# Kernel optimization log

Hardware: AMD Instinct MI355X
Metric: run time of the kernel (lower is better)

## Reference

```python
import jax, jax.numpy as jnp
from jax import lax
import numpy as np

CONF_THRESH = 0.015
NMS_DIST = 4
BORDER = 4
RED = 8


def setup_inputs() -> dict:
    key = jax.random.key(0)
    k1, k2, k3, k4, k5 = jax.random.split(key, 5)
    B, C, H, W = 32, 128, 64, 64
    MID, NCLS = 256, RED * RED + 1
    return {
        "x": jax.random.normal(k1, (B, C, H, W), dtype=jnp.float32),
        "w1": jax.random.normal(k2, (MID, C, 3, 3), dtype=jnp.float32) * 0.05,
        "b1": jax.random.normal(k3, (MID,), dtype=jnp.float32) * 0.05,
        "w2": jax.random.normal(k4, (NCLS, MID, 1, 1), dtype=jnp.float32) * 0.05,
        "b2": jax.random.normal(k5, (NCLS,), dtype=jnp.float32) * 0.05,
    }


def _conv3x3(x, w, b):
    y = lax.conv_general_dilated(
        x, w, window_strides=(1, 1), padding="SAME",
        dimension_numbers=("NCHW", "OIHW", "NCHW"))
    return y + b[None, :, None, None]


def _max_pool(s, r):
    # s: [B, H, W]; infinity-norm neighborhood max, window (2r+1)x(2r+1)
    return lax.reduce_window(
        s, -jnp.inf, lax.max,
        window_dimensions=(1, 2 * r + 1, 2 * r + 1),
        window_strides=(1, 1, 1), padding="SAME")


def _grid_nms(scores, r, iters=8):
    # Iterated local-max suppression; converges to the greedy (sorted-by-score)
    # grid NMS of the original nms_fast routine for distinct scores.
    zeros = jnp.zeros_like(scores)
    max_mask = (scores == _max_pool(scores, r)) & (scores > 0)
    for _ in range(iters):
        supp = _max_pool(max_mask.astype(scores.dtype), r) > 0
        supp_scores = jnp.where(supp, zeros, scores)
        new_max = (supp_scores == _max_pool(supp_scores, r)) & (supp_scores > 0)
        max_mask = max_mask | (new_max & ~supp)
    return jnp.where(max_mask, scores, zeros)


def reference(x, w1, b1, w2, b2):
    B, _, hh, ww = x.shape
    h = jax.nn.relu(_conv3x3(x, w1, b1))                       # [B, mid, hh, ww]
    semi = jnp.einsum("bchw,oc->bohw", h, w2[:, :, 0, 0]) + b2[None, :, None, None]
    dense = jax.nn.softmax(semi, axis=1)                        # [B, 65, hh, ww]
    nodust = dense[:, :-1]                                      # drop dust bin
    # depth-to-space: [B,64,hh,ww] -> [B, hh*8, ww*8]
    heat = nodust.transpose(0, 2, 3, 1).reshape(B, hh, ww, RED, RED)
    heat = heat.transpose(0, 1, 3, 2, 4).reshape(B, hh * RED, ww * RED)
    # confidence threshold
    scores = jnp.where(heat >= CONF_THRESH, heat, 0.0)
    # grid-based NMS (dense keep-map formulation of nms_fast)
    kept = _grid_nms(scores, NMS_DIST)
    # border removal
    Hi, Wi = hh * RED, ww * RED
    yy = jnp.arange(Hi)
    xx = jnp.arange(Wi)
    border = ((yy[:, None] >= BORDER) & (yy[:, None] < Hi - BORDER) &
              (xx[None, :] >= BORDER) & (xx[None, :] < Wi - BORDER))
    return kept * border[None, :, :].astype(kept.dtype)
```

## Files before the change

kernel.cpp:

```cpp
#include <hip/hip_runtime.h>
#include <hip/hip_bf16.h>
#include <stdint.h>

#define BATCH 32
#define CIN 128
#define HH 64
#define WW 64
#define MID 256
#define NCLS 65
#define HI 512
#define NWORDS 8
#define XPS 136
#define HBS2 264
#define SEMS 68

typedef _Float16 half8 __attribute__((ext_vector_type(8)));
typedef _Float16 half4v __attribute__((ext_vector_type(4)));
typedef _Float16 half2v __attribute__((ext_vector_type(2)));
typedef float f32x4 __attribute__((ext_vector_type(4)));

__global__ __launch_bounds__(256) void prep_w1f(
    const float* __restrict__ w1, _Float16* __restrict__ w1fh,
    _Float16* __restrict__ w1fl)
{
    const int idx = blockIdx.x * 256 + threadIdx.x;
    const int j = idx & 7, lane = (idx >> 3) & 63, mt = (idx >> 9) & 15;
    const int s = (idx >> 13) & 3, kix = idx >> 15;
    const int m = mt * 16 + (lane & 15);
    const int c = s * 32 + (lane >> 4) * 8 + j;
    const int ky = kix / 3, kx = kix - ky * 3;
    const float v = w1[((m * CIN + c) * 3 + ky) * 3 + kx];
    const _Float16 hi = (_Float16)v;
    w1fh[idx] = hi;
    w1fl[idx] = (_Float16)(v - (float)hi);
}

__global__ __launch_bounds__(256) void prep_w2f(
    const float* __restrict__ w2, _Float16* __restrict__ w2fh,
    _Float16* __restrict__ w2fl)
{
    const int idx = blockIdx.x * 256 + threadIdx.x;
    const int j = idx & 7, lane = (idx >> 3) & 63;
    const int ks = (idx >> 9) & 7, mt = idx >> 12;
    const int o = mt * 16 + (lane & 15);
    const int k = ks * 32 + (lane >> 4) * 8 + j;
    const float v = (o < NCLS) ? w2[o * MID + k] : 0.f;
    const _Float16 hi = (_Float16)v;
    w2fh[idx] = hi;
    w2fl[idx] = (_Float16)(v - (float)hi);
}

__global__ __launch_bounds__(256) void head_kernel(
    const float* __restrict__ x,
    const _Float16* __restrict__ w1fh, const _Float16* __restrict__ w1fl,
    const _Float16* __restrict__ w2fh, const _Float16* __restrict__ w2fl,
    const float* __restrict__ b1, const float* __restrict__ b2,
    float* __restrict__ out)
{
    const int b  = blockIdx.z;
    const int y0 = blockIdx.y * 8, x0 = blockIdx.x * 8;
    const int tid = threadIdx.x;
    const int lane = tid & 63, w = tid >> 6;
    const int n = lane & 15, q = lane >> 4;

    __shared__ __align__(16) unsigned char SM[54400];
    _Float16* const xh = (_Float16*)SM;
    _Float16* const xl = xh + 100 * XPS;
    _Float16* const hbh = (_Float16*)SM;
    _Float16* const hbl = hbh + 32 * HBS2;
    float* const sem  = (float*)(SM + 33792);
    float* const rinv = sem + 32 * SEMS;

    const float* xb = x + (size_t)b * CIN * HH * WW;
    for (int i = tid; i < 6400; i += 256) {
        const int c2 = i / 100, pos = i - c2 * 100;
        const int r = pos / 10, cc = pos - r * 10;
        const int gy = y0 - 1 + r, gx = x0 - 1 + cc;
        const int c = c2 * 2;
        float v0 = 0.f, v1 = 0.f;
        if ((unsigned)gy < HH && (unsigned)gx < WW) {
            const float* p = xb + (c * HH + gy) * WW + gx;
            v0 = p[0]; v1 = p[HH * WW];
        }
        const _Float16 h0 = (_Float16)v0, h1 = (_Float16)v1;
        half2v hi = {h0, h1};
        half2v lo = {(_Float16)(v0 - (float)h0), (_Float16)(v1 - (float)h1)};
        *(half2v*)(xh + pos * XPS + c) = hi;
        *(half2v*)(xl + pos * XPS + c) = lo;
    }
    __syncthreads();

    f32x4 acc[4][4];
#pragma unroll
    for (int i = 0; i < 4; ++i)
#pragma unroll
        for (int t = 0; t < 4; ++t) acc[i][t] = (f32x4){0.f, 0.f, 0.f, 0.f};

    int bposT[4];
#pragma unroll
    for (int t = 0; t < 4; ++t)
        bposT[t] = (t * 2 + (n >> 3)) * 10 + (n & 7);

    for (int kix = 0; kix < 9; ++kix) {
        const int ky = kix / 3;
        const int koff = ky * 10 + (kix - ky * 3);
#pragma unroll
        for (int s = 0; s < 4; ++s) {
            half8 Ah[4], Al[4];
#pragma unroll
            for (int i = 0; i < 4; ++i) {
                const size_t o = (size_t)(kix * 4 + s) * 8192 +
                                 (w * 4 + i) * 512 + lane * 8;
                Ah[i] = *(const half8*)(w1fh + o);
                Al[i] = *(const half8*)(w1fl + o);
            }
            half8 Bh[4], Bl[4];
#pragma unroll
            for (int t = 0; t < 4; ++t) {
                const int a = (bposT[t] + koff) * XPS + s * 32 + q * 8;
                Bh[t] = *(const half8*)(xh + a);
                Bl[t] = *(const half8*)(xl + a);
            }
#pragma unroll
            for (int i = 0; i < 4; ++i)
#pragma unroll
                for (int t = 0; t < 4; ++t) {
                    acc[i][t] = __builtin_amdgcn_mfma_f32_16x16x32_f16(
                        Ah[i], Bh[t], acc[i][t], 0, 0, 0);
                    acc[i][t] = __builtin_amdgcn_mfma_f32_16x16x32_f16(
                        Ah[i], Bl[t], acc[i][t], 0, 0, 0);
                    acc[i][t] = __builtin_amdgcn_mfma_f32_16x16x32_f16(
                        Al[i], Bh[t], acc[i][t], 0, 0, 0);
                }
        }
    }
    __syncthreads();

    for (int hf = 0; hf < 2; ++hf) {
        if (hf) __syncthreads();
#pragma unroll
        for (int i = 0; i < 4; ++i)
#pragma unroll
            for (int tt = 0; tt < 2; ++tt) {
                const int t = hf * 2 + tt;
                const int p = tt * 16 + n;
                const int m0 = w * 64 + i * 16 + q * 4;
                const f32x4 a = acc[i][t];
                const float4 bv = *(const float4*)(b1 + m0);
                const float h0 = fmaxf(a[0] + bv.x, 0.f);
                const float h1 = fmaxf(a[1] + bv.y, 0.f);
                const float h2 = fmaxf(a[2] + bv.z, 0.f);
                const float h3 = fmaxf(a[3] + bv.w, 0.f);
                half4v hh = {(_Float16)h0, (_Float16)h1,
                             (_Float16)h2, (_Float16)h3};
                half4v hl = {(_Float16)(h0 - (float)hh[0]),
                             (_Float16)(h1 - (float)hh[1]),
                             (_Float16)(h2 - (float)hh[2]),
                             (_Float16)(h3 - (float)hh[3])};
                *(half4v*)(hbh + p * HBS2 + m0) = hh;
                *(half4v*)(hbl + p * HBS2 + m0) = hl;
            }
        __syncthreads();
        {
            const int nt = w & 1;
            const int mt0 = (w < 2) ? 0 : 3;
            const int nmt = (w < 2) ? 3 : 2;
            const int pb = nt * 16 + n;
            f32x4 a2[3];
#pragma unroll
            for (int j = 0; j < 3; ++j) a2[j] = (f32x4){0.f, 0.f, 0.f, 0.f};
#pragma unroll
            for (int ks = 0; ks < 8; ++ks) {
                const int ad = pb * HBS2 + ks * 32 + q * 8;
                const half8 B2h = *(const half8*)(hbh + ad);
                const half8 B2l = *(const half8*)(hbl + ad);
#pragma unroll
                for (int j = 0; j < 3; ++j)
                    if (j < nmt) {
                        const size_t o = (size_t)((mt0 + j) * 8 + ks) * 512 +
                                         lane * 8;
                        const half8 A2h = *(const half8*)(w2fh + o);
                        const half8 A2l = *(const half8*)(w2fl + o);
                        a2[j] = __builtin_amdgcn_mfma_f32_16x16x32_f16(
                            A2h, B2h, a2[j], 0, 0, 0);
                        a2[j] = __builtin_amdgcn_mfma_f32_16x16x32_f16(
                            A2h, B2l, a2[j], 0, 0, 0);
                        a2[j] = __builtin_amdgcn_mfma_f32_16x16x32_f16(
                            A2l, B2h, a2[j], 0, 0, 0);
                    }
            }
#pragma unroll
            for (int j = 0; j < 3; ++j)
                if (j < nmt) {
                    const int o0 = (mt0 + j) * 16 + q * 4;
#pragma unroll
                    for (int r2 = 0; r2 < 4; ++r2) {
                        const int o = o0 + r2;
                        if (o < NCLS)
                            sem[pb * SEMS + o] = a2[j][r2] + b2[o];
                    }
                }
        }
        __syncthreads();
        if (tid < 128) {
            const int p = tid >> 2, q4 = tid & 3;
            const int o0 = q4 * 17;
            const int o1 = (o0 + 17 < NCLS) ? o0 + 17 : NCLS;
            float mx = -1e30f;
            for (int o = o0; o < o1; ++o)
                mx = fmaxf(mx, sem[p * SEMS + o]);
            mx = fmaxf(mx, __shfl_xor(mx, 1));
            mx = fmaxf(mx, __shfl_xor(mx, 2));
            float ssum = 0.f;
            for (int o = o0; o < o1; ++o) {
                float e = __expf(sem[p * SEMS + o] - mx);
                sem[p * SEMS + o] = e;
                ssum += e;
            }
            ssum += __shfl_xor(ssum, 1);
            ssum += __shfl_xor(ssum, 2);
            if (q4 == 0) rinv[p] = 1.f / ssum;
        }
        __syncthreads();
        for (int t2 = tid; t2 < 2048; t2 += 256) {
            const int p = t2 >> 6, o = t2 & 63;
            float v = sem[p * SEMS + o] * rinv[p];
            if (!(v >= 0.015f)) v = 0.f;
            const int P = hf * 32 + p;
            const int py = P >> 3, px = P & 7;
            const int row = (y0 + py) * 8 + (o >> 3);
            const int col = (x0 + px) * 8 + (o & 7);
            out[((size_t)b * HI + row) * HI + col] = v;
        }
    }
}

__global__ __launch_bounds__(256) void nms_iter(
    const float* __restrict__ S, const uint64_t* __restrict__ Min,
    uint64_t* __restrict__ Mout)
{
    const int b = blockIdx.z;
    const int bx = blockIdx.x;
    const int ty = blockIdx.y * 64, tx = bx * 64;
    const int tid = threadIdx.x;

    __shared__ uint64_t smw[80 * 3];
    __shared__ uint64_t hd[80 * 3];
    __shared__ uint64_t sup[72 * 3];
    __shared__ __align__(16) float sfl[72 * 76];
    __shared__ __align__(16) float rm[72 * 64];

    if (tid < 240) {
        const int i = tid / 3, j = tid % 3;
        const int yy = ty - 8 + i;
        const int wj = bx - 1 + j;
        uint64_t v = 0;
        if (Min && (unsigned)yy < HI && (unsigned)wj < NWORDS)
            v = Min[((size_t)b * HI + yy) * NWORDS + wj];
        smw[tid] = v;
    }
    __syncthreads();
    if (tid < 240) {
        const int i = tid / 3, j = tid % 3;
        const uint64_t c = smw[i * 3 + j];
        const uint64_t l = j > 0 ? smw[i * 3 + j - 1] : 0ull;
        const uint64_t r = j < 2 ? smw[i * 3 + j + 1] : 0ull;
        uint64_t d = c;
#pragma unroll
        for (int s = 1; s <= 4; ++s)
            d |= (c >> s) | (r << (64 - s)) | (c << s) | (l >> (64 - s));
        hd[tid] = d;
    }
    __syncthreads();
    if (tid < 216) {
        const int r = tid / 3, j = tid % 3;
        uint64_t v = 0;
#pragma unroll
        for (int k = 0; k < 9; ++k) v |= hd[(r + k) * 3 + j];
        sup[tid] = v;
    }
    __syncthreads();
    const float* Sb = S + (size_t)b * HI * HI;
    for (int k = tid; k < 72 * 18; k += 256) {
        const int r = k / 18, f4 = k % 18;
        const int gy = ty - 4 + r;
        const int gx0 = tx - 4 + f4 * 4;
        float4 v = make_float4(0.f, 0.f, 0.f, 0.f);
        float* pv = (float*)&v;
        if ((unsigned)gy < HI) {
            if (gx0 >= 0 && gx0 + 3 < HI)
                v = *(const float4*)(Sb + (size_t)gy * HI + gx0);
            else {
#pragma unroll
                for (int cc = 0; cc < 4; ++cc)
                    if ((unsigned)(gx0 + cc) < HI)
                        pv[cc] = Sb[(size_t)gy * HI + gx0 + cc];
            }
        }
        const int rel64 = 60 + 4 * f4;
        const uint64_t w = sup[r * 3 + (rel64 >> 6)];
        const int b0 = rel64 & 63;
#pragma unroll
        for (int cc = 0; cc < 4; ++cc)
            if ((w >> (b0 + cc)) & 1ull) pv[cc] = 0.f;
        *(float4*)(sfl + r * 76 + f4 * 4) = v;
    }
    __syncthreads();
    for (int k = tid; k < 72 * 16; k += 256) {
        const int r = k / 16, x4 = (k % 16) * 4;
        const float4 a  = *(const float4*)(sfl + r * 76 + x4);
        const float4 bq = *(const float4*)(sfl + r * 76 + x4 + 4);
        const float4 cq = *(const float4*)(sfl + r * 76 + x4 + 8);
        const float v0=a.x,v1=a.y,v2=a.z,v3=a.w;
        const float v4=bq.x,v5=bq.y,v6=bq.z,v7=bq.w;
        const float v8=cq.x,v9=cq.y,v10=cq.z,v11=cq.w;
        const float m4567 = fmaxf(fmaxf(v4,v5), fmaxf(v6,v7));
        const float m23 = fmaxf(v2,v3), m89 = fmaxf(v8,v9);
        const float o0 = fmaxf(fmaxf(fmaxf(v0,v1), m23), fmaxf(m4567, v8));
        const float o1 = fmaxf(fmaxf(v1, m23), fmaxf(m4567, m89));
        const float o2 = fmaxf(fmaxf(m23, m4567), fmaxf(m89, v10));
        const float o3 = fmaxf(fmaxf(v3, m4567), fmaxf(fmaxf(m89, v10), v11));
        *(float4*)(rm + r * 64 + x4) = make_float4(o0,o1,o2,o3);
    }
    __syncthreads();
    {
        const int wv = tid >> 6, lane = tid & 63;
        const int ybase = wv * 16;
        float ring[9];
#pragma unroll
        for (int k = 0; k < 8; ++k) ring[k] = rm[(ybase + k) * 64 + lane];
#pragma unroll
        for (int qq = 0; qq < 16; ++qq) {
            const int y = ybase + qq;
            ring[(qq + 8) % 9] = rm[(y + 8) * 64 + lane];
            float mv = ring[0];
#pragma unroll
            for (int k = 1; k < 9; ++k) mv = fmaxf(mv, ring[k]);
            const float c = sfl[(y + 4) * 76 + lane + 4];
            const uint64_t oldw = smw[(y + 8) * 3 + 1];
            const bool keep = ((oldw >> lane) & 1ull) || (c == mv && c > 0.f);
            const uint64_t word = __ballot(keep);
            if (lane == 0)
                Mout[((size_t)b * HI + ty + y) * NWORDS + bx] = word;
        }
    }
}

__global__ __launch_bounds__(256) void finalize_bits(
    float* __restrict__ S, const uint64_t* __restrict__ Mw)
{
    const int i4 = blockIdx.x * 256 + threadIdx.x;
    const size_t base = (size_t)i4 * 4;
    const int x = (int)(base & 511);
    const int y = (int)((base >> 9) & 511);
    const int bb = (int)(base >> 18);
    const uint64_t w = Mw[((size_t)bb * HI + y) * NWORDS + (x >> 6)];
    float4 v = ((const float4*)S)[i4];
    float* pv = (float*)&v;
    const bool rowok = (y >= 4) && (y < HI - 4);
#pragma unroll
    for (int cc = 0; cc < 4; ++cc) {
        const int xx = x + cc;
        const bool keep = rowok && (xx >= 4) && (xx < HI - 4) &&
                          ((w >> (xx & 63)) & 1ull);
        if (!keep) pv[cc] = 0.f;
    }
    ((float4*)S)[i4] = v;
}

extern "C" void kernel_launch(void* const* d_in, const int* in_sizes, int n_in,
                              void* d_out, int out_size, void* d_ws, size_t ws_size,
                              hipStream_t stream) {
    const float* x  = (const float*)d_in[0];
    const float* w1 = (const float*)d_in[1];
    const float* b1 = (const float*)d_in[2];
    const float* w2 = (const float*)d_in[3];
    const float* b2 = (const float*)d_in[4];
    float* out = (float*)d_out;

    char* wsb = (char*)d_ws;
    _Float16* w1fh = (_Float16*)(wsb);
    _Float16* w1fl = (_Float16*)(wsb + 0x90000);
    _Float16* w2fh = (_Float16*)(wsb + 0x120000);
    _Float16* w2fl = (_Float16*)(wsb + 0x130000);
    uint64_t* MA   = (uint64_t*)(wsb + 0x140000);
    uint64_t* MB   = (uint64_t*)(wsb + 0x240000);

    prep_w1f<<<294912 / 256, 256, 0, stream>>>(w1, w1fh, w1fl);
    prep_w2f<<<20480 / 256, 256, 0, stream>>>(w2, w2fh, w2fl);
    head_kernel<<<dim3(8, 8, BATCH), 256, 0, stream>>>(
        x, w1fh, w1fl, w2fh, w2fl, b1, b2, out);

    dim3 g(NWORDS, 8, BATCH);
    nms_iter<<<g, 256, 0, stream>>>(out, nullptr, MA);
    for (int it = 0; it < 4; ++it) {
        nms_iter<<<g, 256, 0, stream>>>(out, MA, MB);
        nms_iter<<<g, 256, 0, stream>>>(out, MB, MA);
    }
    const int nf4 = BATCH * HI * HI / 4;
    finalize_bits<<<nf4 / 256, 256, 0, stream>>>(out, MA);
}
```

Measured before the change: 598.6 us.

## Swizzle head input tile in LDS and halve NMS row-max buffer

The head kernel's staged input tile moves from a padded row layout (stride 136 halves) to a 256-byte-per-position layout with an XOR swizzle of 16-byte slots. The aim is to avoid LDS bank conflicts on the half8 B-operand reads and to shrink shared memory from 54400 to 51200 bytes. The NMS iteration kernel now computes the horizontal row-max in two 40-row halves instead of one 72-row pass, cutting the rm buffer from 72x64 to 40x64 floats. That can raise occupancy, at the cost of recomputing 8 overlap rows and adding extra barriers.

```diff
diff --git a/kernel.cpp b/kernel.cpp
--- a/kernel.cpp
+++ b/kernel.cpp
@@ -10,7 +10,6 @@
 #define NCLS 65
 #define HI 512
 #define NWORDS 8
-#define XPS 136
 #define HBS2 264
 #define SEMS 68
 
@@ -63,9 +62,8 @@
     const int lane = tid & 63, w = tid >> 6;
     const int n = lane & 15, q = lane >> 4;
 
-    __shared__ __align__(16) unsigned char SM[54400];
-    _Float16* const xh = (_Float16*)SM;
-    _Float16* const xl = xh + 100 * XPS;
+    __shared__ __align__(16) unsigned char SM[51200];
+    char* const xhb = (char*)SM;
     _Float16* const hbh = (_Float16*)SM;
     _Float16* const hbl = hbh + 32 * HBS2;
     float* const sem  = (float*)(SM + 33792);
@@ -76,17 +74,18 @@
         const int c2 = i / 100, pos = i - c2 * 100;
         const int r = pos / 10, cc = pos - r * 10;
         const int gy = y0 - 1 + r, gx = x0 - 1 + cc;
-        const int c = c2 * 2;
         float v0 = 0.f, v1 = 0.f;
         if ((unsigned)gy < HH && (unsigned)gx < WW) {
-            const float* p = xb + (c * HH + gy) * WW + gx;
+            const float* p = xb + (c2 * 2 * HH + gy) * WW + gx;
             v0 = p[0]; v1 = p[HH * WW];
         }
         const _Float16 h0 = (_Float16)v0, h1 = (_Float16)v1;
         half2v hi = {h0, h1};
         half2v lo = {(_Float16)(v0 - (float)h0), (_Float16)(v1 - (float)h1)};
-        *(half2v*)(xh + pos * XPS + c) = hi;
-        *(half2v*)(xl + pos * XPS + c) = lo;
+        const int slot = (c2 >> 2) ^ (pos & 15);
+        char* p16 = xhb + pos * 256 + (slot << 4) + (c2 & 3) * 4;
+        *(half2v*)p16 = hi;
+        *(half2v*)(p16 + 25600) = lo;
     }
     __syncthreads();
 
@@ -117,9 +116,11 @@
             half8 Bh[4], Bl[4];
 #pragma unroll
             for (int t = 0; t < 4; ++t) {
-                const int a = (bposT[t] + koff) * XPS + s * 32 + q * 8;
-                Bh[t] = *(const half8*)(xh + a);
-                Bl[t] = *(const half8*)(xl + a);
+                const int pos = bposT[t] + koff;
+                const int byteoff = pos * 256 +
+                    ((((s << 2) + q) ^ (pos & 15)) << 4);
+                Bh[t] = *(const half8*)(xhb + byteoff);
+                Bl[t] = *(const half8*)(xhb + 25600 + byteoff);
             }
 #pragma unroll
             for (int i = 0; i < 4; ++i)
@@ -248,7 +249,7 @@
     __shared__ uint64_t hd[80 * 3];
     __shared__ uint64_t sup[72 * 3];
     __shared__ __align__(16) float sfl[72 * 76];
-    __shared__ __align__(16) float rm[72 * 64];
+    __shared__ __align__(16) float rm[40 * 64];
 
     if (tid < 240) {
         const int i = tid / 3, j = tid % 3;
@@ -306,43 +307,50 @@
         *(float4*)(sfl + r * 76 + f4 * 4) = v;
     }
     __syncthreads();
-    for (int k = tid; k < 72 * 16; k += 256) {
-        const int r = k / 16, x4 = (k % 16) * 4;
-        const float4 a  = *(const float4*)(sfl + r * 76 + x4);
-        const float4 bq = *(const float4*)(sfl + r * 76 + x4 + 4);
-        const float4 cq = *(const float4*)(sfl + r * 76 + x4 + 8);
-        const float v0=a.x,v1=a.y,v2=a.z,v3=a.w;
-        const float v4=bq.x,v5=bq.y,v6=bq.z,v7=bq.w;
-        const float v8=cq.x,v9=cq.y,v10=cq.z,v11=cq.w;
-        const float m4567 = fmaxf(fmaxf(v4,v5), fmaxf(v6,v7));
-        const float m23 = fmaxf(v2,v3), m89 = fmaxf(v8,v9);
-        const float o0 = fmaxf(fmaxf(fmaxf(v0,v1), m23), fmaxf(m4567, v8));
-        const float o1 = fmaxf(fmaxf(v1, m23), fmaxf(m4567, m89));
-        const float o2 = fmaxf(fmaxf(m23, m4567), fmaxf(m89, v10));
-        const float o3 = fmaxf(fmaxf(v3, m4567), fmaxf(fmaxf(m89, v10), v11));
-        *(float4*)(rm + r * 64 + x4) = make_float4(o0,o1,o2,o3);
-    }
-    __syncthreads();
-    {
-        const int wv = tid >> 6, lane = tid & 63;
-        const int ybase = wv * 16;
-        float ring[9];
-#pragma unroll
-        for (int k = 0; k < 8; ++k) ring[k] = rm[(ybase + k) * 64 + lane];
-#pragma unroll
-        for (int qq = 0; qq < 16; ++qq) {
-            const int y = ybase + qq;
-            ring[(qq + 8) % 9] = rm[(y + 8) * 64 + lane];
-            float mv = ring[0];
-#pragma unroll
-            for (int k = 1; k < 9; ++k) mv = fmaxf(mv, ring[k]);
-            const float c = sfl[(y + 4) * 76 + lane + 4];
-            const uint64_t oldw = smw[(y + 8) * 3 + 1];
-            const bool keep = ((oldw >> lane) & 1ull) || (c == mv && c > 0.f);
-            const uint64_t word = __ballot(keep);
-            if (lane == 0)
-                Mout[((size_t)b * HI + ty + y) * NWORDS + bx] = word;
-        }
+
+    for (int half = 0; half < 2; ++half) {
+        const int rbase = half * 32;
+        for (int k = tid; k < 40 * 16; k += 256) {
+            const int rr = k / 16, x4 = (k % 16) * 4;
+            const int r = rbase + rr;
+            const float4 a  = *(const float4*)(sfl + r * 76 + x4);
+            const float4 bq = *(const float4*)(sfl + r * 76 + x4 + 4);
+            const float4 cq = *(const float4*)(sfl + r * 76 + x4 + 8);
+            const float v0=a.x,v1=a.y,v2=a.z,v3=a.w;
+            const float v4=bq.x,v5=bq.y,v6=bq.z,v7=bq.w;
+            const float v8=cq.x,v9=cq.y,v10=cq.z,v11=cq.w;
+            const float m4567 = fmaxf(fmaxf(v4,v5), fmaxf(v6,v7));
+            const float m23 = fmaxf(v2,v3), m89 = fmaxf(v8,v9);
+            const float o0 = fmaxf(fmaxf(fmaxf(v0,v1), m23), fmaxf(m4567, v8));
+            const float o1 = fmaxf(fmaxf(v1, m23), fmaxf(m4567, m89));
+            const float o2 = fmaxf(fmaxf(m23, m4567), fmaxf(m89, v10));
+            const float o3 = fmaxf(fmaxf(v3, m4567), fmaxf(fmaxf(m89, v10), v11));
+            *(float4*)(rm + rr * 64 + x4) = make_float4(o0,o1,o2,o3);
+        }
+        __syncthreads();
+        {
+            const int wv = tid >> 6, lane = tid & 63;
+            const int rb = wv * 8;
+            const int ybase = rbase + rb;
+            float ring[9];
+#pragma unroll
+            for (int k = 0; k < 8; ++k) ring[k] = rm[(rb + k) * 64 + lane];
+#pragma unroll
+            for (int qq = 0; qq < 8; ++qq) {
+                const int y = ybase + qq;
+                ring[(qq + 8) % 9] = rm[(rb + qq + 8) * 64 + lane];
+                float mv = ring[0];
+#pragma unroll
+                for (int k = 1; k < 9; ++k) mv = fmaxf(mv, ring[k]);
+                const float c = sfl[(y + 4) * 76 + lane + 4];
+                const uint64_t oldw = smw[(y + 8) * 3 + 1];
+                const bool keep = ((oldw >> lane) & 1ull) || (c == mv && c > 0.f);
+                const uint64_t word = __ballot(keep);
+                if (lane == 0)
+                    Mout[((size_t)b * HI + ty + y) * NWORDS + bx] = word;
+            }
+        }
+        __syncthreads();
     }
 }
 
```

Result: faster. 577.6 us (-3.5%).
